# Performance work log

Measured on AMD Instinct MI355X. Metric: run time of the kernel, lower is better.

The kernel has to match this reference:

```python
import jax, jax.numpy as jnp
import numpy as np

ALPHA, BETA, GAMMA, EPS = 10.0, 0.1, 1.0, 1e-20
MARK_INDEX = jnp.array([0, 29, 88, 117])

B, S, D, P, C, V = 64, 128, 2048, 118, 2, 512


def setup_inputs() -> dict:
    key = jax.random.key(0)
    ks = jax.random.split(key, 9)
    qy_raw = jax.random.uniform(ks[4], (B, S, V), dtype=jnp.float32)
    qy = qy_raw / jnp.sum(qy_raw, axis=-1, keepdims=True)  # probabilities
    return {
        "zs": jax.random.normal(ks[0], (B, S, D), dtype=jnp.float32),
        "rzs": jax.random.normal(ks[1], (B, S, D), dtype=jnp.float32),
        "pts": jax.random.normal(ks[2], (B, S, P, C), dtype=jnp.float32),
        "pts_gt": jax.random.normal(ks[3], (B, S, P, C), dtype=jnp.float32),
        "qy": qy,
        "logits": jax.random.normal(ks[5], (B, S, V), dtype=jnp.float32),
        "best": jax.random.normal(ks[6], (B, P, C), dtype=jnp.float32),
        "best_gt": jax.random.normal(ks[7], (B, P, C), dtype=jnp.float32),
        "mapping": jax.random.randint(ks[8], (B, S), 0, S, dtype=jnp.int64),
        "vector_dims": V,
    }


def _mse(a, b):
    return jnp.mean(jnp.square(a - b))


def reference(zs, rzs, pts, pts_gt, qy, logits, best, best_gt, mapping, vector_dims):
    # KL divergence vs uniform categorical over vector_dims
    log_g = jnp.log(jnp.float32(1.0) / vector_dims)
    kld = jnp.mean(jnp.sum(qy * (jnp.log(qy + EPS) - log_g), axis=-1))

    best_pts_loss = _mse(best, best_gt) + ALPHA * _mse(
        best[..., MARK_INDEX, :], best_gt[..., MARK_INDEX, :]
    )

    # mapping-indexed gather along dim 1 (vectorized form of the double loop;
    # per-element mse means are all over equal-sized slices, so the summed/
    # averaged loop equals a single global mean over the gathered tensors)
    rz_m = jnp.take_along_axis(rzs, mapping[:, :, None], axis=1)          # [B,S,D]
    x_m = jnp.take_along_axis(pts, mapping[:, :, None, None], axis=1)    # [B,S,P,C]
    recon = _mse(rz_m, zs)
    disk = _mse(x_m, pts_gt)
    landmark = _mse(x_m[..., MARK_INDEX, :], pts_gt[..., MARK_INDEX, :])
    pts_loss = disk + ALPHA * landmark

    total = BETA * kld + GAMMA * recon + pts_loss + best_pts_loss
    return total
```

## Files before the change

### kernel.cpp

```cpp
#include <hip/hip_runtime.h>
#include <math.h>

#define NB 64
#define NS 128
#define ND 2048
#define NP 118
#define NC 2
#define NV 512

constexpr int RECON_BLOCKS = 2048;
constexpr int KLD_BLOCKS   = 512;
constexpr int PTS_BLOCKS   = 512;
constexpr int BEST_BLOCKS  = 16;
constexpr int TOTAL_BLOCKS = RECON_BLOCKS + KLD_BLOCKS + PTS_BLOCKS + BEST_BLOCKS;

typedef float f4v __attribute__((ext_vector_type(4)));

__device__ __forceinline__ f4v ntload(const float* p) {
    return __builtin_nontemporal_load((const f4v*)p);
}

__global__ __launch_bounds__(256) void cq_main(
    const float* __restrict__ zs, const float* __restrict__ rzs,
    const float* __restrict__ pts, const float* __restrict__ pts_gt,
    const float* __restrict__ qy,
    const float* __restrict__ best, const float* __restrict__ best_gt,
    const int* __restrict__ mapping, const int* __restrict__ vd,
    float* __restrict__ partials)
{
    const float w_recon = 1.0f / 16777216.0f;
    const float w_kld   = 0.1f / 8192.0f;
    const float w_disk  = 1.0f / 1933312.0f;
    const float w_land  = 10.0f / 65536.0f;
    const float w_best  = 1.0f / 15104.0f;
    const float w_bland = 10.0f / 512.0f;

    const int t   = threadIdx.x;
    const int blk = blockIdx.x;
    float acc = 0.0f;

    __shared__ int mrow[16];

    if (blk < RECON_BLOCKS) {
        const int r0 = blk << 2;
        const int b  = r0 >> 7;
        const int m0 = mapping[r0];
        const int m1 = mapping[r0 + 1];
        const int m2 = mapping[r0 + 2];
        const int m3 = mapping[r0 + 3];
        const float* zb = zs  + ((size_t)r0 << 11);
        const float* rz = rzs + ((size_t)b << 18);
        const size_t rb0 = (size_t)m0 << 11, rb1 = (size_t)m1 << 11;
        const size_t rb2 = (size_t)m2 << 11, rb3 = (size_t)m3 << 11;
        const int e = t << 2;

        f4v z[8], r[8];
        #pragma unroll
        for (int k = 0; k < 8; ++k) z[k] = ntload(zb + ((size_t)k << 10) + e);
        r[0] = ntload(rz + rb0 + e);        r[1] = ntload(rz + rb0 + 1024 + e);
        r[2] = ntload(rz + rb1 + e);        r[3] = ntload(rz + rb1 + 1024 + e);
        r[4] = ntload(rz + rb2 + e);        r[5] = ntload(rz + rb2 + 1024 + e);
        r[6] = ntload(rz + rb3 + e);        r[7] = ntload(rz + rb3 + 1024 + e);

        float s = 0.0f;
        #pragma unroll
        for (int k = 0; k < 8; ++k) {
            f4v d = r[k] - z[k];
            s += d.x*d.x + d.y*d.y + d.z*d.z + d.w*d.w;
        }
        acc = w_recon * s;
    } else if (blk < RECON_BLOCKS + KLD_BLOCKS) {
        const int rb = blk - RECON_BLOCKS;
        const float log_g = -__logf((float)vd[0]);
        const float* qp = qy + ((size_t)rb << 13) + (t << 2);
        f4v q[8];
        #pragma unroll
        for (int k = 0; k < 8; ++k) q[k] = ntload(qp + (k << 10));
        float s = 0.0f;
        #pragma unroll
        for (int k = 0; k < 8; ++k) {
            s += q[k].x * (__logf(q[k].x + 1e-20f) - log_g)
               + q[k].y * (__logf(q[k].y + 1e-20f) - log_g)
               + q[k].z * (__logf(q[k].z + 1e-20f) - log_g)
               + q[k].w * (__logf(q[k].w + 1e-20f) - log_g);
        }
        acc = w_kld * s;
    } else if (blk < RECON_BLOCKS + KLD_BLOCKS + PTS_BLOCKS) {
        const int rb = blk - (RECON_BLOCKS + KLD_BLOCKS);
        if (t < 16) mrow[t] = mapping[(rb << 4) + t];
        __syncthreads();
        const int bs_base = rb << 4;
        f4v x[4], g[4];
        int pbase[4];
        #pragma unroll
        for (int j = 0; j < 4; ++j) {
            const int w = t + j * 256;
            const unsigned rl = (unsigned)w / 59u;
            const int qo = w - (int)rl * 59;
            const bool valid = (w < 944);
            const int rl_c = valid ? (int)rl : 0;
            const int bs = bs_base + rl_c;
            const int b  = bs >> 7;
            const int m  = mrow[rl_c];
            const size_t xi = (size_t)((b << 7) + m) * 236 + (qo << 2);
            const size_t gi = (size_t)(rb * 944 + w) << 2;
            pbase[j] = valid ? (qo << 1) : -100;
            x[j] = valid ? ntload(pts    + xi) : (f4v)(0.0f);
            g[j] = valid ? ntload(pts_gt + gi) : (f4v)(0.0f);
        }
        #pragma unroll
        for (int j = 0; j < 4; ++j) {
            #pragma unroll
            for (int jj = 0; jj < 4; ++jj) {
                const int p = pbase[j] + (jj >> 1);
                const bool marked = (p == 0) | (p == 29) | (p == 88) | (p == 117);
                const float wgt = w_disk + (marked ? w_land : 0.0f);
                const float d = x[j][jj] - g[j][jj];
                acc += wgt * d * d;
            }
        }
    } else {
        const int db = blk - (RECON_BLOCKS + KLD_BLOCKS + PTS_BLOCKS);
        if (t < 236) {
            const int l = db * 236 + t;
            const unsigned bq = (unsigned)l / 59u;
            const int qo = l - (int)bq * 59;
            const f4v x = ntload(best    + ((size_t)l << 2));
            const f4v g = ntload(best_gt + ((size_t)l << 2));
            const int p2 = qo << 1;
            #pragma unroll
            for (int jj = 0; jj < 4; ++jj) {
                const int p = p2 + (jj >> 1);
                const bool marked = (p == 0) | (p == 29) | (p == 88) | (p == 117);
                const float wgt = w_best + (marked ? w_bland : 0.0f);
                const float d = x[jj] - g[jj];
                acc += wgt * d * d;
            }
        }
    }

    #pragma unroll
    for (int o = 32; o > 0; o >>= 1) acc += __shfl_down(acc, o, 64);

    __shared__ float wsum[4];
    if ((t & 63) == 0) wsum[t >> 6] = acc;
    __syncthreads();
    if (t == 0) partials[blk] = wsum[0] + wsum[1] + wsum[2] + wsum[3];
}

__global__ __launch_bounds__(256) void cq_reduce(
    const float* __restrict__ partials, float* __restrict__ out)
{
    const int t = threadIdx.x;
    float acc = 0.0f;
    for (int i = t; i < TOTAL_BLOCKS; i += 256) acc += partials[i];
    #pragma unroll
    for (int o = 32; o > 0; o >>= 1) acc += __shfl_down(acc, o, 64);
    __shared__ float wsum[4];
    if ((t & 63) == 0) wsum[t >> 6] = acc;
    __syncthreads();
    if (t == 0) out[0] = wsum[0] + wsum[1] + wsum[2] + wsum[3];
}

extern "C" void kernel_launch(void* const* d_in, const int* in_sizes, int n_in,
                              void* d_out, int out_size, void* d_ws, size_t ws_size,
                              hipStream_t stream) {
    const float* zs      = (const float*)d_in[0];
    const float* rzs     = (const float*)d_in[1];
    const float* pts     = (const float*)d_in[2];
    const float* pts_gt  = (const float*)d_in[3];
    const float* qy      = (const float*)d_in[4];
    const float* best    = (const float*)d_in[6];
    const float* best_gt = (const float*)d_in[7];
    const int*   mapping = (const int*)d_in[8];
    const int*   vd      = (const int*)d_in[9];
    float* out      = (float*)d_out;
    float* partials = (float*)d_ws;

    cq_main<<<TOTAL_BLOCKS, 256, 0, stream>>>(zs, rzs, pts, pts_gt, qy,
                                              best, best_gt, mapping, vd, partials);
    cq_reduce<<<1, 256, 0, stream>>>(partials, out);
}
```

Before: 177.8 us.

## Fuse final reduction via last-block ticket and use cached loads for gathered rows

Removes the separate single-block reduce kernel. Each block now bumps an atomic ticket after writing its partial, and the last block to arrive sums all partials and writes the output. Adds a memset launch to reset the ticket. The gathered reads of rzs and pts switch from nontemporal to ordinary cached loads, since mapping repeats rows and those rows may be reused from cache.

```diff
diff --git a/kernel.cpp b/kernel.cpp
--- a/kernel.cpp
+++ b/kernel.cpp
@@ -19,6 +19,9 @@
 __device__ __forceinline__ f4v ntload(const float* p) {
     return __builtin_nontemporal_load((const f4v*)p);
 }
+__device__ __forceinline__ f4v cload(const float* p) {
+    return *(const f4v*)p;
+}
 
 __global__ __launch_bounds__(256) void cq_main(
     const float* __restrict__ zs, const float* __restrict__ rzs,
@@ -26,7 +29,8 @@
     const float* __restrict__ qy,
     const float* __restrict__ best, const float* __restrict__ best_gt,
     const int* __restrict__ mapping, const int* __restrict__ vd,
-    float* __restrict__ partials)
+    float* __restrict__ partials, unsigned int* __restrict__ ticket,
+    float* __restrict__ out)
 {
     const float w_recon = 1.0f / 16777216.0f;
     const float w_kld   = 0.1f / 8192.0f;
@@ -57,10 +61,10 @@
         f4v z[8], r[8];
         #pragma unroll
         for (int k = 0; k < 8; ++k) z[k] = ntload(zb + ((size_t)k << 10) + e);
-        r[0] = ntload(rz + rb0 + e);        r[1] = ntload(rz + rb0 + 1024 + e);
-        r[2] = ntload(rz + rb1 + e);        r[3] = ntload(rz + rb1 + 1024 + e);
-        r[4] = ntload(rz + rb2 + e);        r[5] = ntload(rz + rb2 + 1024 + e);
-        r[6] = ntload(rz + rb3 + e);        r[7] = ntload(rz + rb3 + 1024 + e);
+        r[0] = cload(rz + rb0 + e);        r[1] = cload(rz + rb0 + 1024 + e);
+        r[2] = cload(rz + rb1 + e);        r[3] = cload(rz + rb1 + 1024 + e);
+        r[4] = cload(rz + rb2 + e);        r[5] = cload(rz + rb2 + 1024 + e);
+        r[6] = cload(rz + rb3 + e);        r[7] = cload(rz + rb3 + 1024 + e);
 
         float s = 0.0f;
         #pragma unroll
@@ -105,7 +109,7 @@
             const size_t xi = (size_t)((b << 7) + m) * 236 + (qo << 2);
             const size_t gi = (size_t)(rb * 944 + w) << 2;
             pbase[j] = valid ? (qo << 1) : -100;
-            x[j] = valid ? ntload(pts    + xi) : (f4v)(0.0f);
+            x[j] = valid ? cload(pts     + xi) : (f4v)(0.0f);
             g[j] = valid ? ntload(pts_gt + gi) : (f4v)(0.0f);
         }
         #pragma unroll
@@ -143,23 +147,27 @@
     for (int o = 32; o > 0; o >>= 1) acc += __shfl_down(acc, o, 64);
 
     __shared__ float wsum[4];
+    __shared__ int lastflag;
     if ((t & 63) == 0) wsum[t >> 6] = acc;
     __syncthreads();
-    if (t == 0) partials[blk] = wsum[0] + wsum[1] + wsum[2] + wsum[3];
-}
+    if (t == 0) {
+        partials[blk] = wsum[0] + wsum[1] + wsum[2] + wsum[3];
+        __threadfence();
+        unsigned old = atomicAdd(ticket, 1u);
+        lastflag = (old == (unsigned)(TOTAL_BLOCKS - 1));
+    }
+    __syncthreads();
 
-__global__ __launch_bounds__(256) void cq_reduce(
-    const float* __restrict__ partials, float* __restrict__ out)
-{
-    const int t = threadIdx.x;
-    float acc = 0.0f;
-    for (int i = t; i < TOTAL_BLOCKS; i += 256) acc += partials[i];
-    #pragma unroll
-    for (int o = 32; o > 0; o >>= 1) acc += __shfl_down(acc, o, 64);
-    __shared__ float wsum[4];
-    if ((t & 63) == 0) wsum[t >> 6] = acc;
-    __syncthreads();
-    if (t == 0) out[0] = wsum[0] + wsum[1] + wsum[2] + wsum[3];
+    if (lastflag) {
+        float a2 = 0.0f;
+        for (int i = t; i < TOTAL_BLOCKS; i += 256)
+            a2 += atomicAdd(&partials[i], 0.0f);
+        #pragma unroll
+        for (int o = 32; o > 0; o >>= 1) a2 += __shfl_down(a2, o, 64);
+        if ((t & 63) == 0) wsum[t >> 6] = a2;
+        __syncthreads();
+        if (t == 0) out[0] = wsum[0] + wsum[1] + wsum[2] + wsum[3];
+    }
 }
 
 extern "C" void kernel_launch(void* const* d_in, const int* in_sizes, int n_in,
@@ -176,8 +184,11 @@
     const int*   vd      = (const int*)d_in[9];
     float* out      = (float*)d_out;
     float* partials = (float*)d_ws;
+    unsigned int* ticket = (unsigned int*)((char*)d_ws + TOTAL_BLOCKS * sizeof(float));
+
+    hipMemsetAsync(ticket, 0, sizeof(unsigned int), stream);
 
     cq_main<<<TOTAL_BLOCKS, 256, 0, stream>>>(zs, rzs, pts, pts_gt, qy,
-                                              best, best_gt, mapping, vd, partials);
-    cq_reduce<<<1, 256, 0, stream>>>(partials, out);
+                                              best, best_gt, mapping, vd,
+                                              partials, ticket, out);
 }
```

Measured after the change: 328.7 us. 84.9% more time.
